# Optimization experiments

Hardware: AMD Instinct MI355X
Metric: run time of the kernel (lower is better)

Reference implementation:

```python
import jax, jax.numpy as jnp
import numpy as np

B, S, D = 64, 1024, 256
N_HEADS = 1
HEAD_DIM = D // N_HEADS
MASK_VAL = -10000.0


def setup_inputs() -> dict:
    key = jax.random.key(0)
    k1, k2, k3 = jax.random.split(key, 3)
    x = jax.random.normal(k1, (B, S, D), dtype=jnp.float32)
    W_qkv = jax.random.normal(k2, (D, 3 * D), dtype=jnp.float32) * 0.02
    b_qkv = jnp.zeros((3 * D,), dtype=jnp.float32)
    W_out = jax.random.normal(k3, (D, D), dtype=jnp.float32) * 0.02
    b_out = jnp.zeros((D,), dtype=jnp.float32)
    return {"x": x, "W_qkv": W_qkv, "b_qkv": b_qkv, "W_out": W_out, "b_out": b_out}


def reference(x, W_qkv, b_qkv, W_out, b_out):
    # QKV projection: [B,S,3D]
    qkv = jnp.einsum('bsd,df->bsf', x, W_qkv) + b_qkv
    q, k, v = jnp.split(qkv, 3, axis=2)
    # split heads -> [B,H,S,hd] (H=1)
    def split_heads(t):
        return t.reshape(B, S, N_HEADS, HEAD_DIM).transpose(0, 2, 1, 3)
    q, k, v = split_heads(q), split_heads(k), split_heads(v)
    # scaled scores [B,H,S,S]
    scores = jnp.einsum('bhqd,bhkd->bhqk', q, k) / jnp.sqrt(jnp.float32(HEAD_DIM))
    causal = jnp.tril(jnp.ones((1, 1, S, S), dtype=bool))
    scores = jnp.where(causal, scores, jnp.float32(MASK_VAL))
    attn = jax.nn.softmax(scores, axis=-1)  # dropout deterministic (training=False)
    out = jnp.einsum('bhqk,bhkd->bhqd', attn, v)
    # merge heads -> [B,S,D]
    out = out.transpose(0, 2, 1, 3).reshape(B, S, D)
    out = jnp.einsum('bsd,de->bse', out, W_out) + b_out
    return out, attn
```

## Files before the change

kernel.cpp:

```cpp
#include <hip/hip_runtime.h>
#include <hip/hip_bf16.h>

#define BB 64
#define SS 1024
#define DDIM 256

typedef unsigned short u16;
typedef __attribute__((ext_vector_type(4))) float f4;
typedef __attribute__((ext_vector_type(8))) short bf16x8;
typedef __attribute__((ext_vector_type(4))) short bf16x4;
typedef __attribute__((ext_vector_type(4))) float f32x4;

__device__ inline u16 f2b(float f) {
  unsigned int u = __float_as_uint(f);
  unsigned int r = (u + 0x7fffu + ((u >> 16) & 1u)) >> 16;
  return (u16)r;
}

#define GLOAD16(g, l)                                                  \
  __builtin_amdgcn_global_load_lds(                                    \
      (const __attribute__((address_space(1))) void*)(g),              \
      (__attribute__((address_space(3))) void*)(l), 16, 0, 0)

__global__ __launch_bounds__(256) void cast_x(const float* __restrict__ x,
                                              u16* __restrict__ xb, int n8) {
  int i = blockIdx.x * 256 + threadIdx.x;
  const int stride = gridDim.x * 256;
  for (; i < n8; i += stride) {
    f4 a = ((const f4*)x)[2 * i];
    f4 b = ((const f4*)x)[2 * i + 1];
    bf16x8 o;
    o[0] = f2b(a[0]); o[1] = f2b(a[1]); o[2] = f2b(a[2]); o[3] = f2b(a[3]);
    o[4] = f2b(b[0]); o[5] = f2b(b[1]); o[6] = f2b(b[2]); o[7] = f2b(b[3]);
    ((bf16x8*)xb)[i] = o;
  }
}

__global__ __launch_bounds__(256) void cast_w(const float* __restrict__ Wqkv,
                                              const float* __restrict__ Wout,
                                              u16* __restrict__ Wqkvt,
                                              u16* __restrict__ Woutt) {
  int t = blockIdx.x * 256 + threadIdx.x;
  if (t < 256 * 768) {
    int k = t / 768, n = t % 768;
    Wqkvt[n * 256 + k] = f2b(Wqkv[t]);
  }
  if (t < 256 * 256) {
    int k = t / 256, n = t % 256;
    Woutt[n * 256 + k] = f2b(Wout[t]);
  }
}

template <int EPI, int NXT>
__global__ __launch_bounds__(256) void gemm_mfma(
    const u16* __restrict__ A, const u16* __restrict__ Bt,
    const float* __restrict__ bias, float* __restrict__ outF,
    u16* __restrict__ Qb, u16* __restrict__ Kb, u16* __restrict__ Vt) {
  __shared__ u16 As[128 * 64];
  __shared__ u16 Bs[128 * 64];
  const int t = threadIdx.x;
  const int w = t >> 6, l = t & 63;
  const int lr = l & 15, lg = l >> 4;
  const int id = blockIdx.x;
  const int r8 = id & 7;
  const int tt = id >> 3;
  const int xt = tt % NXT;
  const int yt = (tt / NXT) * 8 + r8;
  const int m0 = yt * 128, n0 = xt * 128;
  const int wm = (w >> 1) * 64, wn = (w & 1) * 64;

  f32x4 acc[4][4] = {};

  const int srow = w * 8 + (l >> 3);
  const int csrc = (l & 7) ^ (srow & 7);

  for (int k0 = 0; k0 < 256; k0 += 64) {
    __syncthreads();
#pragma unroll
    for (int i = 0; i < 4; ++i) {
      const int row = i * 32 + srow;
      GLOAD16(&A[(size_t)(m0 + row) * 256 + k0 + csrc * 8],
              &As[(i * 32 + w * 8) * 64]);
      GLOAD16(&Bt[(size_t)(n0 + row) * 256 + k0 + csrc * 8],
              &Bs[(i * 32 + w * 8) * 64]);
    }
    __syncthreads();
#pragma unroll
    for (int kc = 0; kc < 2; ++kc) {
      bf16x8 af[4], bfr[4];
#pragma unroll
      for (int f = 0; f < 4; ++f) {
        int ar = wm + f * 16 + lr;
        af[f] = *(const bf16x8*)&As[ar * 64 + (((kc * 4 + lg) ^ (ar & 7)) * 8)];
        int br = wn + f * 16 + lr;
        bfr[f] = *(const bf16x8*)&Bs[br * 64 + (((kc * 4 + lg) ^ (br & 7)) * 8)];
      }
#pragma unroll
      for (int i = 0; i < 4; ++i)
#pragma unroll
        for (int jn = 0; jn < 4; ++jn)
          acc[i][jn] = __builtin_amdgcn_mfma_f32_16x16x32_bf16(
              af[i], bfr[jn], acc[i][jn], 0, 0, 0);
    }
  }

#pragma unroll
  for (int i = 0; i < 4; ++i) {
    const int mbase = m0 + wm + i * 16 + lg * 4;
#pragma unroll
    for (int jn = 0; jn < 4; ++jn) {
      const int n = n0 + wn + jn * 16 + lr;
      const float bv = bias[n];
      if (EPI == 0) {
#pragma unroll
        for (int r = 0; r < 4; ++r)
          outF[(size_t)(mbase + r) * 256 + n] = acc[i][jn][r] + bv;
      } else {
        if (n < 256) {
#pragma unroll
          for (int r = 0; r < 4; ++r)
            Qb[(size_t)(mbase + r) * 256 + n] = f2b(acc[i][jn][r] + bv);
        } else if (n < 512) {
#pragma unroll
          for (int r = 0; r < 4; ++r)
            Kb[(size_t)(mbase + r) * 256 + (n - 256)] = f2b(acc[i][jn][r] + bv);
        } else {
          const int d = n - 512;
          const int b = mbase >> 10, sl = mbase & 1023;
          bf16x4 pk;
#pragma unroll
          for (int r = 0; r < 4; ++r) pk[r] = f2b(acc[i][jn][r] + bv);
          *(bf16x4*)&Vt[((size_t)b * 256 + d) * 1024 + sl] = pk;
        }
      }
    }
  }
}

__global__ __launch_bounds__(256) void attn_fused(
    const u16* __restrict__ Qg, const u16* __restrict__ Kg,
    const u16* __restrict__ Vtg, float* __restrict__ attn,
    u16* __restrict__ outa) {
  __shared__ u16 pool[35328];
  u16* Ks = pool;
  u16* Vs = pool + 16384;
  u16* Ps = pool + 32768;

  const int t = threadIdx.x;
  const int w = t >> 6, l = t & 63;
  const int lr = l & 15, lg = l >> 4;
  const int id = blockIdx.x;
  const int b = (id & 7) * 8 + ((id >> 3) & 7);
  const int pair = id >> 6;
  const int qta = pair, qtb = 15 - pair;

  const u16* Kbase = Kg + (size_t)b * SS * DDIM;
  const u16* Vbase = Vtg + (size_t)b * DDIM * SS;

  auto stageK = [&](int kt, int buf) {
    const int rbase = 8 * w;
#pragma unroll
    for (int i = 0; i < 4; ++i) {
      const int rr = rbase + 2 * i + (l >> 5);
      const int chunk = l & 31;
      const int csrc = (chunk & 24) | ((chunk & 7) ^ (rr & 7));
      const u16* g = Kbase + (size_t)(kt * 32 + rr) * DDIM + csrc * 8;
      GLOAD16(g, Ks + buf * 8192 + (rbase + 2 * i) * 256);
    }
  };
  auto stageV = [&](int kt, int buf) {
    const int dbase = 64 * w;
    const int dd = dbase + (l >> 2);
    const u16* g0 = Vbase + (size_t)dd * SS + kt * 32 + (l & 3) * 8;
#pragma unroll
    for (int i = 0; i < 4; ++i)
      GLOAD16(g0 + (size_t)16 * i * SS, Vs + buf * 8192 + (dbase + 16 * i) * 32);
  };
  auto loadQ = [&](int qt, bf16x8* qf) {
    const u16* qb = Qg + ((size_t)(b * SS + qt * 64 + w * 16 + lr)) * DDIM;
#pragma unroll
    for (int kc = 0; kc < 8; ++kc)
      qf[kc] = *(const bf16x8*)&qb[kc * 32 + lg * 8];
  };

  bf16x8 qfA[8], qfB[8];
  loadQ(qta, qfA);
  loadQ(qtb, qfB);
  const int lastA = 2 * qta + 1, lastB = 2 * qtb + 1;
  float raA[4] = {0.f, 0.f, 0.f, 0.f}, raB[4] = {0.f, 0.f, 0.f, 0.f};

  stageK(0, 0);
  __syncthreads();
  for (int kt = 0; kt <= lastB; ++kt) {
    const int buf = kt & 1;
    if (kt < lastB) stageK(kt + 1, buf ^ 1);
    const bool doA = (kt <= lastA);
#pragma unroll
    for (int sf = 0; sf < 2; ++sf) {
      const int srow = sf * 16 + lr;
      const u16* kr = Ks + buf * 8192 + srow * 256;
      f32x4 sA = {0.f, 0.f, 0.f, 0.f}, sB = {0.f, 0.f, 0.f, 0.f};
#pragma unroll
      for (int kc = 0; kc < 8; ++kc) {
        const int c = kc * 4 + lg;
        const int ch = (c & 24) | ((c & 7) ^ (srow & 7));
        bf16x8 bfr = *(const bf16x8*)&kr[ch * 8];
        sB = __builtin_amdgcn_mfma_f32_16x16x32_bf16(qfB[kc], bfr, sB, 0, 0, 0);
        if (doA)
          sA = __builtin_amdgcn_mfma_f32_16x16x32_bf16(qfA[kc], bfr, sA, 0, 0, 0);
      }
      const int scol = kt * 32 + sf * 16 + lr;
      {
        const int qrow = qtb * 64 + w * 16 + lg * 4;
#pragma unroll
        for (int r = 0; r < 4; ++r)
          raB[r] += (scol <= qrow + r) ? __expf(sB[r] * 0.0625f) : 0.f;
      }
      if (doA) {
        const int qrow = qta * 64 + w * 16 + lg * 4;
#pragma unroll
        for (int r = 0; r < 4; ++r)
          raA[r] += (scol <= qrow + r) ? __expf(sA[r] * 0.0625f) : 0.f;
      }
    }
    __syncthreads();
  }
#pragma unroll
  for (int m = 1; m < 16; m <<= 1) {
#pragma unroll
    for (int r = 0; r < 4; ++r) {
      raA[r] += __shfl_xor(raA[r], m, 64);
      raB[r] += __shfl_xor(raB[r], m, 64);
    }
  }
  float invA[4], invB[4];
#pragma unroll
  for (int r = 0; r < 4; ++r) {
    invA[r] = 1.0f / raA[r];
    invB[r] = 1.0f / raB[r];
  }

  for (int tile = 0; tile < 2; ++tile) {
    const int qt = tile ? qtb : qta;
    const int last = 2 * qt + 1;
    bf16x8 qf[8];
    loadQ(qt, qf);
    float inv[4];
#pragma unroll
    for (int r = 0; r < 4; ++r) inv[r] = tile ? invB[r] : invA[r];
    f32x4 oacc[16];
#pragma unroll
    for (int df = 0; df < 16; ++df) oacc[df] = (f32x4){0.f, 0.f, 0.f, 0.f};

    float* attnw = attn + ((size_t)(b * SS + qt * 64 + w * 16)) * SS;

    __syncthreads();
    stageK(0, 0);
    stageV(0, 0);
    __syncthreads();

    for (int kt = 0; kt <= last; ++kt) {
      const int buf = kt & 1;
      if (kt < last) {
        stageK(kt + 1, buf ^ 1);
        stageV(kt + 1, buf ^ 1);
      }
#pragma unroll
      for (int sf = 0; sf < 2; ++sf) {
        const int srow = sf * 16 + lr;
        const u16* kr = Ks + buf * 8192 + srow * 256;
        f32x4 s = {0.f, 0.f, 0.f, 0.f};
#pragma unroll
        for (int kc = 0; kc < 8; ++kc) {
          const int c = kc * 4 + lg;
          const int ch = (c & 24) | ((c & 7) ^ (srow & 7));
          bf16x8 bfr = *(const bf16x8*)&kr[ch * 8];
          s = __builtin_amdgcn_mfma_f32_16x16x32_bf16(qf[kc], bfr, s, 0, 0, 0);
        }
        const int scol = kt * 32 + sf * 16 + lr;
        const int qrow = qt * 64 + w * 16 + lg * 4;
#pragma unroll
        for (int r = 0; r < 4; ++r) {
          const float e = (scol <= qrow + r) ? __expf(s[r] * 0.0625f) : 0.f;
          Ps[(w * 16 + lg * 4 + r) * 40 + sf * 16 + lr] = f2b(e * inv[r]);
        }
      }
#pragma unroll
      for (int g2 = 0; g2 < 2; ++g2) {
        const int row = g2 * 8 + (l >> 3);
        const int col = (l & 7) * 4;
        bf16x4 pv = *(const bf16x4*)&Ps[(w * 16 + row) * 40 + col];
        f4 o;
#pragma unroll
        for (int j = 0; j < 4; ++j)
          o[j] = __uint_as_float(((unsigned)(u16)pv[j]) << 16);
        *(f4*)&attnw[(size_t)row * SS + kt * 32 + col] = o;
      }
      {
        bf16x8 pa = *(const bf16x8*)&Ps[(w * 16 + lr) * 40 + lg * 8];
        const u16* vb = Vs + buf * 8192;
#pragma unroll
        for (int df = 0; df < 16; ++df) {
          bf16x8 vfr = *(const bf16x8*)&vb[(df * 16 + lr) * 32 + lg * 8];
          oacc[df] = __builtin_amdgcn_mfma_f32_16x16x32_bf16(pa, vfr, oacc[df],
                                                            0, 0, 0);
        }
      }
      __syncthreads();
    }

    {
      const f4 z = {0.f, 0.f, 0.f, 0.f};
      for (int c0 = (qt + 1) * 64; c0 < SS; c0 += 32) {
#pragma unroll
        for (int g2 = 0; g2 < 2; ++g2) {
          const int row = g2 * 8 + (l >> 3);
          *(f4*)&attnw[(size_t)row * SS + c0 + (l & 7) * 4] = z;
        }
      }
    }

    __syncthreads();
#pragma unroll
    for (int df = 0; df < 16; ++df)
#pragma unroll
      for (int r = 0; r < 4; ++r)
        pool[(w * 16 + lg * 4 + r) * 264 + df * 16 + lr] = f2b(oacc[df][r]);
    {
      const size_t obase = (size_t)(b * SS + qt * 64);
#pragma unroll
      for (int i = 0; i < 8; ++i) {
        const int row = w * 16 + 2 * i + (l >> 5);
        bf16x8 v = *(const bf16x8*)&pool[row * 264 + (l & 31) * 8];
        *(bf16x8*)&outa[(obase + row) * DDIM + (l & 31) * 8] = v;
      }
    }
  }
}

extern "C" void kernel_launch(void* const* d_in, const int* in_sizes, int n_in,
                              void* d_out, int out_size, void* d_ws,
                              size_t ws_size, hipStream_t stream) {
  const float* x    = (const float*)d_in[0];
  const float* Wqkv = (const float*)d_in[1];
  const float* bqkv = (const float*)d_in[2];
  const float* Wout = (const float*)d_in[3];
  const float* bout = (const float*)d_in[4];

  float* out  = (float*)d_out;
  float* attn = out + (size_t)BB * SS * DDIM;

  const size_t NTOK = (size_t)BB * SS;
  u16* ws = (u16*)d_ws;
  u16* xb    = ws;
  u16* Qb    = xb + NTOK * DDIM;
  u16* Kb    = Qb + NTOK * DDIM;
  u16* Vt    = Kb + NTOK * DDIM;
  u16* outa  = Vt + NTOK * DDIM;
  u16* Wqkvt = outa + NTOK * DDIM;
  u16* Woutt = Wqkvt + 768 * 256;

  cast_x<<<2048, 256, 0, stream>>>(x, xb, (int)(NTOK * DDIM / 8));
  cast_w<<<768, 256, 0, stream>>>(Wqkv, Wout, Wqkvt, Woutt);

  gemm_mfma<1, 6><<<3072, 256, 0, stream>>>(xb, Wqkvt, bqkv, nullptr, Qb, Kb,
                                            Vt);
  attn_fused<<<512, 256, 0, stream>>>(Qb, Kb, Vt, attn, outa);
  gemm_mfma<0, 2><<<1024, 256, 0, stream>>>(outa, Woutt, bout, out, nullptr,
                                            nullptr, nullptr);
}
```

Baseline: 272.4 us.

## Process both causal query tiles in one K/V sweep sharing staged tiles

```diff
diff --git a/kernel.cpp b/kernel.cpp
--- a/kernel.cpp
+++ b/kernel.cpp
@@ -137,14 +137,15 @@
   }
 }
 
-__global__ __launch_bounds__(256) void attn_fused(
+__global__ __launch_bounds__(256, 2) void attn_fused(
     const u16* __restrict__ Qg, const u16* __restrict__ Kg,
     const u16* __restrict__ Vtg, float* __restrict__ attn,
     u16* __restrict__ outa) {
-  __shared__ u16 pool[35328];
-  u16* Ks = pool;
-  u16* Vs = pool + 16384;
-  u16* Ps = pool + 32768;
+  __shared__ u16 pool[37888];
+  u16* Ks  = pool;
+  u16* Vs  = pool + 16384;
+  u16* PsA = pool + 32768;
+  u16* PsB = pool + 35328;
 
   const int t = threadIdx.x;
   const int w = t >> 6, l = t & 63;
@@ -240,100 +241,137 @@
     invB[r] = 1.0f / raB[r];
   }
 
-  for (int tile = 0; tile < 2; ++tile) {
-    const int qt = tile ? qtb : qta;
-    const int last = 2 * qt + 1;
-    bf16x8 qf[8];
-    loadQ(qt, qf);
-    float inv[4];
-#pragma unroll
-    for (int r = 0; r < 4; ++r) inv[r] = tile ? invB[r] : invA[r];
-    f32x4 oacc[16];
-#pragma unroll
-    for (int df = 0; df < 16; ++df) oacc[df] = (f32x4){0.f, 0.f, 0.f, 0.f};
-
-    float* attnw = attn + ((size_t)(b * SS + qt * 64 + w * 16)) * SS;
-
-    __syncthreads();
-    stageK(0, 0);
-    stageV(0, 0);
-    __syncthreads();
-
-    for (int kt = 0; kt <= last; ++kt) {
-      const int buf = kt & 1;
-      if (kt < last) {
-        stageK(kt + 1, buf ^ 1);
-        stageV(kt + 1, buf ^ 1);
-      }
-#pragma unroll
-      for (int sf = 0; sf < 2; ++sf) {
-        const int srow = sf * 16 + lr;
-        const u16* kr = Ks + buf * 8192 + srow * 256;
-        f32x4 s = {0.f, 0.f, 0.f, 0.f};
-#pragma unroll
-        for (int kc = 0; kc < 8; ++kc) {
-          const int c = kc * 4 + lg;
-          const int ch = (c & 24) | ((c & 7) ^ (srow & 7));
-          bf16x8 bfr = *(const bf16x8*)&kr[ch * 8];
-          s = __builtin_amdgcn_mfma_f32_16x16x32_bf16(qf[kc], bfr, s, 0, 0, 0);
+  f32x4 oaccA[16], oaccB[16];
+#pragma unroll
+  for (int df = 0; df < 16; ++df) {
+    oaccA[df] = (f32x4){0.f, 0.f, 0.f, 0.f};
+    oaccB[df] = (f32x4){0.f, 0.f, 0.f, 0.f};
+  }
+  float* attnA = attn + ((size_t)(b * SS + qta * 64 + w * 16)) * SS;
+  float* attnB = attn + ((size_t)(b * SS + qtb * 64 + w * 16)) * SS;
+
+  stageK(0, 0);
+  stageV(0, 0);
+  __syncthreads();
+
+  for (int kt = 0; kt <= lastB; ++kt) {
+    const int buf = kt & 1;
+    if (kt < lastB) {
+      stageK(kt + 1, buf ^ 1);
+      stageV(kt + 1, buf ^ 1);
+    }
+    const bool doA = (kt <= lastA);
+#pragma unroll
+    for (int sf = 0; sf < 2; ++sf) {
+      const int srow = sf * 16 + lr;
+      const u16* kr = Ks + buf * 8192 + srow * 256;
+      f32x4 sA = {0.f, 0.f, 0.f, 0.f}, sB = {0.f, 0.f, 0.f, 0.f};
+#pragma unroll
+      for (int kc = 0; kc < 8; ++kc) {
+        const int c = kc * 4 + lg;
+        const int ch = (c & 24) | ((c & 7) ^ (srow & 7));
+        bf16x8 bfr = *(const bf16x8*)&kr[ch * 8];
+        sB = __builtin_amdgcn_mfma_f32_16x16x32_bf16(qfB[kc], bfr, sB, 0, 0, 0);
+        if (doA)
+          sA = __builtin_amdgcn_mfma_f32_16x16x32_bf16(qfA[kc], bfr, sA, 0, 0, 0);
+      }
+      const int scol = kt * 32 + sf * 16 + lr;
+      {
+        const int qrow = qtb * 64 + w * 16 + lg * 4;
+#pragma unroll
+        for (int r = 0; r < 4; ++r) {
+          const float e = (scol <= qrow + r) ? __expf(sB[r] * 0.0625f) : 0.f;
+          PsB[(w * 16 + lg * 4 + r) * 40 + sf * 16 + lr] = f2b(e * invB[r]);
         }
-        const int scol = kt * 32 + sf * 16 + lr;
-        const int qrow = qt * 64 + w * 16 + lg * 4;
+      }
+      if (doA) {
+        const int qrow = qta * 64 + w * 16 + lg * 4;
 #pragma unroll
         for (int r = 0; r < 4; ++r) {
-          const float e = (scol <= qrow + r) ? __expf(s[r] * 0.0625f) : 0.f;
-          Ps[(w * 16 + lg * 4 + r) * 40 + sf * 16 + lr] = f2b(e * inv[r]);
+          const float e = (scol <= qrow + r) ? __expf(sA[r] * 0.0625f) : 0.f;
+          PsA[(w * 16 + lg * 4 + r) * 40 + sf * 16 + lr] = f2b(e * invA[r]);
         }
       }
+    }
+#pragma unroll
+    for (int g2 = 0; g2 < 2; ++g2) {
+      const int row = g2 * 8 + (l >> 3);
+      const int col = (l & 7) * 4;
+      bf16x4 pv = *(const bf16x4*)&PsB[(w * 16 + row) * 40 + col];
+      f4 o;
+#pragma unroll
+      for (int j = 0; j < 4; ++j)
+        o[j] = __uint_as_float(((unsigned)(u16)pv[j]) << 16);
+      *(f4*)&attnB[(size_t)row * SS + kt * 32 + col] = o;
+    }
+    if (doA) {
 #pragma unroll
       for (int g2 = 0; g2 < 2; ++g2) {
         const int row = g2 * 8 + (l >> 3);
         const int col = (l & 7) * 4;
-        bf16x4 pv = *(const bf16x4*)&Ps[(w * 16 + row) * 40 + col];
+        bf16x4 pv = *(const bf16x4*)&PsA[(w * 16 + row) * 40 + col];
         f4 o;
 #pragma unroll
         for (int j = 0; j < 4; ++j)
           o[j] = __uint_as_float(((unsigned)(u16)pv[j]) << 16);
-        *(f4*)&attnw[(size_t)row * SS + kt * 32 + col] = o;
-      }
-      {
-        bf16x8 pa = *(const bf16x8*)&Ps[(w * 16 + lr) * 40 + lg * 8];
-        const u16* vb = Vs + buf * 8192;
+        *(f4*)&attnA[(size_t)row * SS + kt * 32 + col] = o;
+      }
+    }
+    {
+      const u16* vb = Vs + buf * 8192;
+      bf16x8 paB = *(const bf16x8*)&PsB[(w * 16 + lr) * 40 + lg * 8];
+#pragma unroll
+      for (int df = 0; df < 16; ++df) {
+        bf16x8 vfr = *(const bf16x8*)&vb[(df * 16 + lr) * 32 + lg * 8];
+        oaccB[df] = __builtin_amdgcn_mfma_f32_16x16x32_bf16(paB, vfr,
+                                                            oaccB[df], 0, 0, 0);
+      }
+      if (doA) {
+        bf16x8 paA = *(const bf16x8*)&PsA[(w * 16 + lr) * 40 + lg * 8];
 #pragma unroll
         for (int df = 0; df < 16; ++df) {
           bf16x8 vfr = *(const bf16x8*)&vb[(df * 16 + lr) * 32 + lg * 8];
-          oacc[df] = __builtin_amdgcn_mfma_f32_16x16x32_bf16(pa, vfr, oacc[df],
-                                                            0, 0, 0);
+          oaccA[df] = __builtin_amdgcn_mfma_f32_16x16x32_bf16(
+              paA, vfr, oaccA[df], 0, 0, 0);
         }
       }
-      __syncthreads();
-    }
-
-    {
-      const f4 z = {0.f, 0.f, 0.f, 0.f};
-      for (int c0 = (qt + 1) * 64; c0 < SS; c0 += 32) {
-#pragma unroll
-        for (int g2 = 0; g2 < 2; ++g2) {
-          const int row = g2 * 8 + (l >> 3);
-          *(f4*)&attnw[(size_t)row * SS + c0 + (l & 7) * 4] = z;
-        }
-      }
-    }
-
+    }
     __syncthreads();
+  }
+
+  {
+    const f4 z = {0.f, 0.f, 0.f, 0.f};
+    for (int c0 = (qta + 1) * 64; c0 < SS; c0 += 32) {
+#pragma unroll
+      for (int g2 = 0; g2 < 2; ++g2) {
+        const int row = g2 * 8 + (l >> 3);
+        *(f4*)&attnA[(size_t)row * SS + c0 + (l & 7) * 4] = z;
+      }
+    }
+    for (int c0 = (qtb + 1) * 64; c0 < SS; c0 += 32) {
+#pragma unroll
+      for (int g2 = 0; g2 < 2; ++g2) {
+        const int row = g2 * 8 + (l >> 3);
+        *(f4*)&attnB[(size_t)row * SS + c0 + (l & 7) * 4] = z;
+      }
+    }
+  }
+
+#pragma unroll
+  for (int tile = 0; tile < 2; ++tile) {
+    const int qt = tile ? qtb : qta;
 #pragma unroll
     for (int df = 0; df < 16; ++df)
 #pragma unroll
       for (int r = 0; r < 4; ++r)
-        pool[(w * 16 + lg * 4 + r) * 264 + df * 16 + lr] = f2b(oacc[df][r]);
-    {
-      const size_t obase = (size_t)(b * SS + qt * 64);
-#pragma unroll
-      for (int i = 0; i < 8; ++i) {
-        const int row = w * 16 + 2 * i + (l >> 5);
-        bf16x8 v = *(const bf16x8*)&pool[row * 264 + (l & 31) * 8];
-        *(bf16x8*)&outa[(obase + row) * DDIM + (l & 31) * 8] = v;
-      }
+        pool[(w * 16 + lg * 4 + r) * 264 + df * 16 + lr] =
+            f2b(tile ? oaccB[df][r] : oaccA[df][r]);
+    const size_t obase = (size_t)(b * SS + qt * 64);
+#pragma unroll
+    for (int i = 0; i < 8; ++i) {
+      const int row = w * 16 + 2 * i + (l >> 5);
+      bf16x8 v = *(const bf16x8*)&pool[row * 264 + (l & 31) * 8];
+      *(bf16x8*)&outa[(obase + row) * DDIM + (l & 31) * 8] = v;
     }
   }
 }
```

After: 411.3 us. 1.51x slower.
